# Optimization experiments

Measured on AMD Instinct MI355X. Metric: run time of the kernel, lower is better.

## Reference

```python
import jax, jax.numpy as jnp
import numpy as np

N_NODES = 40000
N_EDGES = 640000
HIDDEN = 128
N_LAYERS = 4
N_CLASSES = 40
SCALING = HIDDEN ** -0.5  # num_heads = 1 -> head_dim = HIDDEN


def setup_inputs() -> dict:
    key = jax.random.key(0)
    ks = jax.random.split(key, 8)
    w_scale = HIDDEN ** -0.5
    h = jax.random.normal(ks[0], (N_NODES, HIDDEN), dtype=jnp.float32)
    src = jax.random.randint(ks[1], (N_EDGES,), 0, N_NODES, dtype=jnp.int32)
    dst = jnp.sort(jax.random.randint(ks[2], (N_EDGES,), 0, N_NODES, dtype=jnp.int32))
    Wq = jax.random.normal(ks[3], (N_LAYERS, HIDDEN, HIDDEN), dtype=jnp.float32) * w_scale
    Wk = jax.random.normal(ks[4], (N_LAYERS, HIDDEN, HIDDEN), dtype=jnp.float32) * w_scale
    Wv = jax.random.normal(ks[5], (N_LAYERS, HIDDEN, HIDDEN), dtype=jnp.float32) * w_scale
    bq = jnp.zeros((N_LAYERS, HIDDEN), dtype=jnp.float32)
    bk = jnp.zeros((N_LAYERS, HIDDEN), dtype=jnp.float32)
    bv = jnp.zeros((N_LAYERS, HIDDEN), dtype=jnp.float32)
    Wout = jax.random.normal(ks[6], (HIDDEN, N_CLASSES), dtype=jnp.float32) * w_scale
    bout = jnp.zeros((N_CLASSES,), dtype=jnp.float32)
    return {"h": h, "src": src, "dst": dst, "Wq": Wq, "bq": bq, "Wk": Wk,
            "bk": bk, "Wv": Wv, "bv": bv, "Wout": Wout, "bout": bout}


def _edge_softmax_spmm(q, k, v, src, dst):
    """Sparse MHA over graph edges (num_heads=1).
    score_e = <q[dst_e], k[src_e]>, softmax over incoming edges per dst,
    out[i] = sum_{e: dst_e = i} attn_e * v[src_e].
    """
    # SDDMM: [E]
    score = jnp.einsum('ed,ed->e', q[dst], k[src])
    # edge softmax over destination segments (stable)
    m = jax.ops.segment_max(score, dst, num_segments=N_NODES)  # [N]
    e = jnp.exp(score - m[dst])                                # [E]
    s = jax.ops.segment_sum(e, dst, num_segments=N_NODES)      # [N]
    attn = e / jnp.maximum(s[dst], 1e-20)                      # [E]
    # SpMM: [N, d]
    return jax.ops.segment_sum(attn[:, None] * v[src], dst, num_segments=N_NODES)


def reference(h, src, dst, Wq, bq, Wk, bk, Wv, bv, Wout, bout):
    for l in range(N_LAYERS):
        q = (h @ Wq[l] + bq[l]) * SCALING
        k = h @ Wk[l] + bk[l]
        v = h @ Wv[l] + bv[l]
        h = _edge_softmax_spmm(q, k, v, src, dst)
    logits = h @ Wout + bout
    return jax.nn.log_softmax(logits, axis=-1)
```

## Files before the change

kernel.cpp:

```cpp
#include <hip/hip_runtime.h>
#include <math.h>

#define N_NODES 40000
#define N_EDGES 640000
#define HIDDEN 128
#define N_LAYERS 4
#define N_CLASSES 40
#define SCALING 0.08838834764831845f

typedef __attribute__((ext_vector_type(8))) short short8;
typedef __attribute__((ext_vector_type(4))) float floatx4;

static __device__ __forceinline__ float b2f(unsigned short u) {
  return __uint_as_float(((unsigned)u) << 16);
}
static __device__ __forceinline__ unsigned short f2b(float f) {
  unsigned u = __float_as_uint(f);
  u += 0x7fff + ((u >> 16) & 1);
  return (unsigned short)(u >> 16);
}

struct MMJob {
  const float* A; const float* B;
  float* Cf; unsigned short* Cb;
  float scale;
  int abt; int ncolsB; int storeT; int padrows;
};
struct MM7 { MMJob j[7]; };
struct MM3 { MMJob j[3]; };

static __device__ __forceinline__ void run_job(const MMJob J, int bi) {
  int ty = threadIdx.x >> 7;
  int c  = threadIdx.x & 127;
  int r  = bi * 2 + ty;
  float acc = 0.f;
  if (J.abt) {
    const float* ar = J.A + (size_t)r * 128;
    const float* br = J.B + (size_t)c * 128;
    #pragma unroll 4
    for (int j = 0; j < 128; ++j) acc += ar[j] * br[j];
  } else if (c < J.ncolsB) {
    const float* ar = J.A + (size_t)r * 128;
    #pragma unroll 4
    for (int j = 0; j < 128; ++j) acc += ar[j] * J.B[(size_t)j * J.ncolsB + c];
  }
  acc *= J.scale;
  if (J.storeT) {
    if (c < J.ncolsB) {
      if (J.Cb) J.Cb[(size_t)c * 128 + r] = f2b(acc);
      else      J.Cf[(size_t)c * 128 + r] = acc;
    } else if (c < J.padrows && J.Cb) {
      J.Cb[(size_t)c * 128 + r] = 0;
    }
  } else if (c < J.ncolsB) {
    if (J.Cb) J.Cb[(size_t)r * J.ncolsB + c] = f2b(acc);
    else      J.Cf[(size_t)r * J.ncolsB + c] = acc;
  }
}

__global__ __launch_bounds__(256) void setup_fold1(
    const float* __restrict__ h_in, const int* __restrict__ dst,
    const float* __restrict__ bq, const float* __restrict__ Wk,
    unsigned short* __restrict__ g0, int* __restrict__ row_start,
    float* __restrict__ zb, MM7 st)
{
  int blk = blockIdx.x;
  if (blk < 2657) {
    int idx = blk * 256 + threadIdx.x;
    if (idx < 640000) {
      const float4* p = (const float4*)h_in + (size_t)idx * 2;
      float4 a = p[0], b = p[1];
      union { unsigned short us[8]; uint4 v; } o;
      o.us[0] = f2b(a.x); o.us[1] = f2b(a.y); o.us[2] = f2b(a.z); o.us[3] = f2b(a.w);
      o.us[4] = f2b(b.x); o.us[5] = f2b(b.y); o.us[6] = f2b(b.z); o.us[7] = f2b(b.w);
      ((uint4*)g0)[idx] = o.v;
      return;
    }
    int c = idx - 640000;
    if (c <= N_NODES) {
      int lo = 0, hi = N_EDGES;
      while (lo < hi) {
        int mid = (lo + hi) >> 1;
        if (dst[mid] < c) lo = mid + 1; else hi = mid;
      }
      row_start[c] = lo;
    }
    return;
  }
  if (blk < 3105) {
    int b2 = blk - 2657;
    run_job(st.j[b2 >> 6], b2 & 63);
    return;
  }
  int t = threadIdx.x;
  if (t < 128) {
    const float* wkr = Wk + (size_t)t * 128;
    float s = 0.f;
    #pragma unroll 4
    for (int o = 0; o < 128; ++o) s += bq[o] * wkr[o];
    zb[t] = s * SCALING;
  }
}

__global__ __launch_bounds__(256) void fold2(MM7 st) {
  run_job(st.j[blockIdx.x >> 6], blockIdx.x & 63);
}

__global__ __launch_bounds__(256) void fold3_z0(
    MM3 st,
    const float* __restrict__ Wq, const float* __restrict__ Wk,
    const float* __restrict__ Wv, const float* __restrict__ Wout,
    const float* __restrict__ bq, const float* __restrict__ bv,
    const float* __restrict__ bout,
    const float* __restrict__ D01, const float* __restrict__ C3f,
    float* __restrict__ zb, float* __restrict__ bout2,
    const unsigned short* __restrict__ g, const unsigned short* __restrict__ WZ0,
    unsigned short* __restrict__ zout)
{
  int blk = blockIdx.x;
  if (blk < 192) {
    run_job(st.j[blk >> 6], blk & 63);
    return;
  }
  if (blk == 192) {
    int t = threadIdx.x;
    __shared__ float cb[128], v1[128], v2[128], cbn[128];
    if (t < 128) cb[t] = bv[t];
    __syncthreads();
    for (int l = 1; l < 4; ++l) {
      const float* Cvl = (l == 1) ? Wv : (l == 2 ? D01 : C3f);
      if (t < 128) {
        float s = bq[(size_t)l * 128 + t];
        for (int o = 0; o < 128; ++o) s += cb[o] * Wq[(size_t)l * 16384 + (size_t)o * 128 + t];
        v1[t] = s;
      }
      __syncthreads();
      if (t < 128) {
        float s = 0.f;
        const float* wkr = Wk + (size_t)l * 16384 + (size_t)t * 128;
        for (int o = 0; o < 128; ++o) s += v1[o] * wkr[o];
        v2[t] = s;
      }
      __syncthreads();
      if (t < 128) {
        float s = 0.f;
        const float* cvr = Cvl + (size_t)t * 128;
        for (int d = 0; d < 128; ++d) s += v2[d] * cvr[d];
        zb[(size_t)l * 128 + t] = s * SCALING;
        float s2 = bv[(size_t)l * 128 + t];
        for (int d = 0; d < 128; ++d) s2 += cb[d] * Wv[(size_t)l * 16384 + (size_t)d * 128 + t];
        cbn[t] = s2;
      }
      __syncthreads();
      if (t < 128) cb[t] = cbn[t];
      __syncthreads();
    }
    if (t < N_CLASSES) {
      float s = bout[t];
      for (int d = 0; d < 128; ++d) s += cb[d] * Wout[(size_t)d * N_CLASSES + t];
      bout2[t] = s;
    }
    return;
  }

  {
    const int tile = blk - 193;
    constexpr int ROWB = 256;
    __shared__ __align__(16) unsigned char cs[32 * ROWB];

    const int tid = threadIdx.x;
    const int wid = tid >> 6, lane = tid & 63;
    const int r = lane & 15, kg = lane >> 4;
    const int colhalf = wid & 1, rowsub = wid >> 1;
    const int colbase = colhalf * 64;
    const int ro = rowsub * 16 + r;
    const int row = tile * 32 + ro;

    short8 hf[4];
    #pragma unroll
    for (int kc = 0; kc < 4; ++kc)
      hf[kc] = *(const short8*)(g + (size_t)row * 128 + kc * 32 + kg * 8);

    floatx4 acc[4];
    #pragma unroll
    for (int df = 0; df < 4; ++df) acc[df] = (floatx4){0.f, 0.f, 0.f, 0.f};

    const unsigned short* wp = WZ0 + (size_t)(colbase + r) * 128 + kg * 8;
    #pragma unroll
    for (int df = 0; df < 4; ++df) {
      #pragma unroll
      for (int kc = 0; kc < 4; ++kc) {
        short8 wf = *(const short8*)(wp + df * 2048 + kc * 32);
        acc[df] = __builtin_amdgcn_mfma_f32_16x16x32_bf16(wf, hf[kc], acc[df], 0, 0, 0);
      }
    }

    #pragma unroll
    for (int df = 0; df < 4; ++df) {
      float4 b4 = *(const float4*)&zb[colbase + df * 16 + kg * 4];
      union { unsigned short us[4]; uint2 u2; } o;
      o.us[0] = f2b(acc[df][0] + b4.x);
      o.us[1] = f2b(acc[df][1] + b4.y);
      o.us[2] = f2b(acc[df][2] + b4.z);
      o.us[3] = f2b(acc[df][3] + b4.w);
      int colb = (colbase + df * 16 + kg * 4) * 2;
      *(uint2*)(cs + ro * ROWB + (colb ^ ((ro & 7) << 4))) = o.u2;
    }
    __syncthreads();

    unsigned char* dstb = (unsigned char*)(zout + (size_t)tile * 32 * 128);
    #pragma unroll
    for (int i = 0; i < 2; ++i) {
      int byte = (i * 256 + tid) * 16;
      int ro2 = byte / ROWB;
      int colb2 = byte & (ROWB - 1);
      *(uint4*)(dstb + byte) =
          *(const uint4*)(cs + ro2 * ROWB + (colb2 ^ ((ro2 & 7) << 4)));
    }
  }
}

__global__ __launch_bounds__(256) void gemm_z(
    const unsigned short* __restrict__ A,
    const unsigned short* __restrict__ Wt,
    const float* __restrict__ bias,
    unsigned short* __restrict__ C)
{
  constexpr int ROWB = 256;
  __shared__ __align__(16) unsigned char cs[32 * ROWB];

  const int tid = threadIdx.x;
  const int wid = tid >> 6, lane = tid & 63;
  const int r = lane & 15, kg = lane >> 4;
  const int colhalf = wid & 1, rowsub = wid >> 1;
  const int colbase = colhalf * 64;
  const int ro = rowsub * 16 + r;
  const int row = blockIdx.x * 32 + ro;

  short8 hf[4];
  #pragma unroll
  for (int kc = 0; kc < 4; ++kc)
    hf[kc] = *(const short8*)(A + (size_t)row * 128 + kc * 32 + kg * 8);

  floatx4 acc[4];
  #pragma unroll
  for (int df = 0; df < 4; ++df) acc[df] = (floatx4){0.f, 0.f, 0.f, 0.f};

  const unsigned short* wp = Wt + (size_t)(colbase + r) * 128 + kg * 8;
  #pragma unroll
  for (int df = 0; df < 4; ++df) {
    #pragma unroll
    for (int kc = 0; kc < 4; ++kc) {
      short8 wf = *(const short8*)(wp + df * 2048 + kc * 32);
      acc[df] = __builtin_amdgcn_mfma_f32_16x16x32_bf16(wf, hf[kc], acc[df], 0, 0, 0);
    }
  }

  #pragma unroll
  for (int df = 0; df < 4; ++df) {
    float4 b4 = *(const float4*)&bias[colbase + df * 16 + kg * 4];
    union { unsigned short us[4]; uint2 u2; } o;
    o.us[0] = f2b(acc[df][0] + b4.x);
    o.us[1] = f2b(acc[df][1] + b4.y);
    o.us[2] = f2b(acc[df][2] + b4.z);
    o.us[3] = f2b(acc[df][3] + b4.w);
    int colb = (colbase + df * 16 + kg * 4) * 2;
    *(uint2*)(cs + ro * ROWB + (colb ^ ((ro & 7) << 4))) = o.u2;
  }
  __syncthreads();

  unsigned char* dstb = (unsigned char*)(C + (size_t)blockIdx.x * 32 * 128);
  #pragma unroll
  for (int i = 0; i < 2; ++i) {
    int byte = (i * 256 + tid) * 16;
    int ro2 = byte / ROWB;
    int colb2 = byte & (ROWB - 1);
    *(uint4*)(dstb + byte) =
        *(const uint4*)(cs + ro2 * ROWB + (colb2 ^ ((ro2 & 7) << 4)));
  }
}

#define EDGE_LOADG(VLD, HF, C)                                          \
  {                                                                     \
    int e_ = (C) + sg;                                                  \
    VLD = e_ < r1;                                                      \
    int s_ = VLD ? src[e_] : 0;                                         \
    HF = *(const short8*)(g + ((size_t)s_ << 7) + sl * 8);              \
  }

#define EDGE_COMPG(VLD, HF)                                             \
  {                                                                     \
    float hd_[8];                                                       \
    _Pragma("unroll")                                                   \
    for (int j = 0; j < 8; ++j) hd_[j] = b2f((unsigned short)HF[j]);    \
    float d0_ = 0.f, d1_ = 0.f;                                         \
    _Pragma("unroll")                                                   \
    for (int j = 0; j < 4; ++j) d0_ += qd[j] * hd_[j];                  \
    _Pragma("unroll")                                                   \
    for (int j = 4; j < 8; ++j) d1_ += qd[j] * hd_[j];                  \
    float d_ = d0_ + d1_;                                               \
    d_ += __shfl_xor(d_, 1, 64);                                        \
    d_ += __shfl_xor(d_, 2, 64);                                        \
    d_ += __shfl_xor(d_, 4, 64);                                        \
    d_ += __shfl_xor(d_, 8, 64);                                        \
    float w_ = VLD ? __expf(d_) : 0.f;                                  \
    ws += w_;                                                           \
    _Pragma("unroll")                                                   \
    for (int j = 0; j < 8; ++j) acc[j] += w_ * hd_[j];                  \
  }

#define EDGE_BODY                                                       \
  float acc[8] = {0.f, 0.f, 0.f, 0.f, 0.f, 0.f, 0.f, 0.f};              \
  float ws = 0.f;                                                       \
  bool vA, vB;                                                          \
  short8 hA, hB;                                                        \
  EDGE_LOADG(vA, hA, r0);                                               \
  EDGE_LOADG(vB, hB, r0 + 4);                                           \
  for (int c = r0; c < r1; c += 8) {                                    \
    bool vC, vD;                                                        \
    short8 hC, hD;                                                      \
    EDGE_LOADG(vC, hC, c + 8);                                          \
    EDGE_LOADG(vD, hD, c + 12);                                         \
    EDGE_COMPG(vA, hA);                                                 \
    EDGE_COMPG(vB, hB);                                                 \
    vA = vC; hA = hC;                                                   \
    vB = vD; hB = hD;                                                   \
  }                                                                     \
  _Pragma("unroll")                                                     \
  for (int off = 16; off <= 32; off <<= 1) {                            \
    ws += __shfl_xor(ws, off, 64);                                      \
    _Pragma("unroll")                                                   \
    for (int j = 0; j < 8; ++j) acc[j] += __shfl_xor(acc[j], off, 64);  \
  }

__global__ __launch_bounds__(128) void edge_fused(
    const unsigned short* __restrict__ z, const unsigned short* __restrict__ g,
    const int* __restrict__ src, const int* __restrict__ row_start,
    unsigned short* __restrict__ gout)
{
  const int lane = threadIdx.x & 63;
  const int node = blockIdx.x * 2 + (threadIdx.x >> 6);
  const int sg = lane >> 4, sl = lane & 15;

  short8 qf = *(const short8*)(z + ((size_t)node << 7) + sl * 8);
  float qd[8];
  #pragma unroll
  for (int j = 0; j < 8; ++j) qd[j] = b2f((unsigned short)qf[j]);

  const int r0 = row_start[node], r1 = row_start[node + 1];

  EDGE_BODY

  if (sg == 0) {
    float inv = (ws > 1e-20f) ? 1.0f / ws : 0.0f;
    union { unsigned short us[8]; uint4 u4; } o;
    #pragma unroll
    for (int j = 0; j < 8; ++j) o.us[j] = f2b(acc[j] * inv);
    *(uint4*)(gout + (size_t)node * 128 + sl * 8) = o.u4;
  }
}

__global__ __launch_bounds__(128) void edge_head(
    const unsigned short* __restrict__ z, const unsigned short* __restrict__ g,
    const int* __restrict__ src, const int* __restrict__ row_start,
    const unsigned short* __restrict__ WOt, const float* __restrict__ bout2,
    float* __restrict__ out)
{
  const int lane = threadIdx.x & 63;
  const int node = blockIdx.x * 2 + (threadIdx.x >> 6);
  const int sg = lane >> 4, sl = lane & 15;

  short8 qf = *(const short8*)(z + ((size_t)node << 7) + sl * 8);
  float qd[8];
  #pragma unroll
  for (int j = 0; j < 8; ++j) qd[j] = b2f((unsigned short)qf[j]);

  const int r0 = row_start[node], r1 = row_start[node + 1];

  EDGE_BODY

  float inv = (ws > 1e-20f) ? 1.0f / ws : 0.0f;

  float cls[10];
  #pragma unroll
  for (int it = 0; it < 10; ++it) {
    int c = sg * 10 + it;
    short8 w = *(const short8*)(WOt + (size_t)c * 128 + sl * 8);
    float p = 0.f;
    #pragma unroll
    for (int j = 0; j < 8; ++j) p += acc[j] * b2f((unsigned short)w[j]);
    p += __shfl_xor(p, 1, 64);
    p += __shfl_xor(p, 2, 64);
    p += __shfl_xor(p, 4, 64);
    p += __shfl_xor(p, 8, 64);
    cls[it] = p * inv + bout2[c];
  }
  float m = cls[0];
  #pragma unroll
  for (int it = 1; it < 10; ++it) m = fmaxf(m, cls[it]);
  m = fmaxf(m, __shfl_xor(m, 16, 64));
  m = fmaxf(m, __shfl_xor(m, 32, 64));
  float s = 0.f;
  #pragma unroll
  for (int it = 0; it < 10; ++it) s += __expf(cls[it] - m);
  s += __shfl_xor(s, 16, 64);
  s += __shfl_xor(s, 32, 64);
  float lse = m + logf(s);

  if (sl < 10) {
    float v = cls[0];
    #pragma unroll
    for (int it = 1; it < 10; ++it) if (sl == it) v = cls[it];
    out[(size_t)node * N_CLASSES + sg * 10 + sl] = v - lse;
  }
}

#undef EDGE_BODY
#undef EDGE_COMPG
#undef EDGE_LOADG

extern "C" void kernel_launch(void* const* d_in, const int* in_sizes, int n_in,
                              void* d_out, int out_size, void* d_ws, size_t ws_size,
                              hipStream_t stream) {
  const float* h_in = (const float*)d_in[0];
  const int*   src  = (const int*)d_in[1];
  const int*   dst  = (const int*)d_in[2];
  const float* Wq   = (const float*)d_in[3];
  const float* bq   = (const float*)d_in[4];
  const float* Wk   = (const float*)d_in[5];
  const float* bk   = (const float*)d_in[6];
  const float* Wv   = (const float*)d_in[7];
  const float* bv   = (const float*)d_in[8];
  const float* Wout = (const float*)d_in[9];
  const float* bout = (const float*)d_in[10];
  float* out = (float*)d_out;
  (void)bk;

  char* ws = (char*)d_ws;
  size_t off = 0;
  auto alloc = [&](size_t bytes) -> void* {
    void* p = ws + off;
    off += (bytes + 255) & ~(size_t)255;
    return p;
  };
  int*            row_start = (int*)           alloc((size_t)(N_NODES + 1) * sizeof(int));
  unsigned short* g0        = (unsigned short*)alloc((size_t)N_NODES * 128 * 2);
  unsigned short* g1        = (unsigned short*)alloc((size_t)N_NODES * 128 * 2);
  unsigned short* zbuf      = (unsigned short*)alloc((size_t)N_NODES * 128 * 2);
  unsigned short* WZ        = (unsigned short*)alloc((size_t)4 * 16384 * 2);
  unsigned short* WOt       = (unsigned short*)alloc((size_t)48 * 128 * 2);
  float*          D01  = (float*)alloc(16384 * 4);
  float*          D23  = (float*)alloc(16384 * 4);
  float*          A1f  = (float*)alloc(16384 * 4);
  float*          B1f  = (float*)alloc(16384 * 4);
  float*          E3   = (float*)alloc(16384 * 4);
  float*          F3   = (float*)alloc(16384 * 4);
  float*          A2f  = (float*)alloc(16384 * 4);
  float*          B2f  = (float*)alloc(16384 * 4);
  float*          A3f  = (float*)alloc(16384 * 4);
  float*          B3f  = (float*)alloc(16384 * 4);
  float*          C4f  = (float*)alloc(16384 * 4);
  float*          C3f  = (float*)alloc(16384 * 4);
  float*          zb   = (float*)alloc(4 * 128 * 4);
  float*          bout2 = (float*)alloc(64 * 4);

  auto J = [](const float* A, const float* B, float* Cf, unsigned short* Cb,
              float scale, int abt, int ncolsB, int storeT, int padrows) {
    MMJob j; j.A = A; j.B = B; j.Cf = Cf; j.Cb = Cb; j.scale = scale;
    j.abt = abt; j.ncolsB = ncolsB; j.storeT = storeT; j.padrows = padrows;
    return j;
  };
  const float* Wq_l[4] = {Wq, Wq + 16384, Wq + 32768, Wq + 49152};
  const float* Wk_l[4] = {Wk, Wk + 16384, Wk + 32768, Wk + 49152};
  const float* Wv_l[4] = {Wv, Wv + 16384, Wv + 32768, Wv + 49152};

  MM7 s1;
  s1.j[0] = J(Wk_l[0], Wq_l[0], nullptr, WZ, SCALING, 1, 128, 0, 0);
  s1.j[1] = J(Wv_l[0], Wv_l[1], D01, nullptr, 1.f, 0, 128, 0, 0);
  s1.j[2] = J(Wv_l[2], Wv_l[3], D23, nullptr, 1.f, 0, 128, 0, 0);
  s1.j[3] = J(Wv_l[0], Wk_l[1], A1f, nullptr, 1.f, 0, 128, 0, 0);
  s1.j[4] = J(Wv_l[0], Wq_l[1], B1f, nullptr, 1.f, 0, 128, 0, 0);
  s1.j[5] = J(Wv_l[2], Wk_l[3], E3,  nullptr, 1.f, 0, 128, 0, 0);
  s1.j[6] = J(Wv_l[2], Wq_l[3], F3,  nullptr, 1.f, 0, 128, 0, 0);

  MM7 s2;
  s2.j[0] = J(A1f, B1f, nullptr, WZ + 16384, SCALING, 1, 128, 0, 0);
  s2.j[1] = J(D01, Wk_l[2], A2f, nullptr, 1.f, 0, 128, 0, 0);
  s2.j[2] = J(D01, Wq_l[2], B2f, nullptr, 1.f, 0, 128, 0, 0);
  s2.j[3] = J(D01, E3, A3f, nullptr, 1.f, 0, 128, 0, 0);
  s2.j[4] = J(D01, F3, B3f, nullptr, 1.f, 0, 128, 0, 0);
  s2.j[5] = J(D01, D23, C4f, nullptr, 1.f, 0, 128, 0, 0);
  s2.j[6] = J(D01, Wv_l[2], C3f, nullptr, 1.f, 0, 128, 0, 0);

  MM3 s3;
  s3.j[0] = J(A2f, B2f, nullptr, WZ + 32768, SCALING, 1, 128, 0, 0);
  s3.j[1] = J(A3f, B3f, nullptr, WZ + 49152, SCALING, 1, 128, 0, 0);
  s3.j[2] = J(C4f, Wout, nullptr, WOt, 1.f, 0, N_CLASSES, 1, 48);

  setup_fold1<<<3106, 256, 0, stream>>>(h_in, dst, bq, Wk, g0, row_start, zb, s1);
  fold2<<<448, 256, 0, stream>>>(s2);
  fold3_z0<<<1443, 256, 0, stream>>>(s3, Wq, Wk, Wv, Wout, bq, bv, bout,
                                     D01, C3f, zb, bout2, g0, WZ, zbuf);

  edge_fused<<<N_NODES / 2, 128, 0, stream>>>(zbuf, g0, src, row_start, g1);
  gemm_z<<<1250, 256, 0, stream>>>(g1, WZ + 16384, zb + 128, zbuf);
  edge_fused<<<N_NODES / 2, 128, 0, stream>>>(zbuf, g1, src, row_start, g0);
  gemm_z<<<1250, 256, 0, stream>>>(g0, WZ + 32768, zb + 256, zbuf);
  edge_fused<<<N_NODES / 2, 128, 0, stream>>>(zbuf, g0, src, row_start, g1);
  gemm_z<<<1250, 256, 0, stream>>>(g1, WZ + 49152, zb + 384, zbuf);
  edge_head<<<N_NODES / 2, 128, 0, stream>>>(zbuf, g1, src, row_start, WOt, bout2, out);
}
```

Baseline: 241.5 us.

## Split output head into separate MFMA kernel and fold log2e into scores

Replaces the fused edge_head kernel, which did the per-node 128x40 output projection with scalar dot products and shuffles, with a plain edge_fused pass followed by a separate MFMA bf16 GEMM kernel that also computes log-softmax and writes through shared memory. The log2(e) factor is folded into the score-projection scales so the edge kernel can call exp2f instead of __expf. This costs one extra kernel launch and a bf16 round trip of the final hidden state through global memory. In exchange the class projection moves onto matrix cores and the edge loop does slightly less work per edge.

```diff
diff --git a/kernel.cpp b/kernel.cpp
--- a/kernel.cpp
+++ b/kernel.cpp
@@ -7,6 +7,7 @@
 #define N_LAYERS 4
 #define N_CLASSES 40
 #define SCALING 0.08838834764831845f
+#define LOG2E 1.4426950408889634f
 
 typedef __attribute__((ext_vector_type(8))) short short8;
 typedef __attribute__((ext_vector_type(4))) float floatx4;
@@ -98,7 +99,7 @@
     float s = 0.f;
     #pragma unroll 4
     for (int o = 0; o < 128; ++o) s += bq[o] * wkr[o];
-    zb[t] = s * SCALING;
+    zb[t] = s * (SCALING * LOG2E);
   }
 }
 
@@ -146,7 +147,7 @@
         float s = 0.f;
         const float* cvr = Cvl + (size_t)t * 128;
         for (int d = 0; d < 128; ++d) s += v2[d] * cvr[d];
-        zb[(size_t)l * 128 + t] = s * SCALING;
+        zb[(size_t)l * 128 + t] = s * (SCALING * LOG2E);
         float s2 = bv[(size_t)l * 128 + t];
         for (int d = 0; d < 128; ++d) s2 += cb[d] * Wv[(size_t)l * 16384 + (size_t)d * 128 + t];
         cbn[t] = s2;
@@ -280,7 +281,26 @@
   }
 }
 
-#define EDGE_LOADG(VLD, HF, C)                                          \
+__global__ __launch_bounds__(128) void edge_fused(
+    const unsigned short* __restrict__ z, const unsigned short* __restrict__ g,
+    const int* __restrict__ src, const int* __restrict__ row_start,
+    unsigned short* __restrict__ gout)
+{
+  const int lane = threadIdx.x & 63;
+  const int node = blockIdx.x * 2 + (threadIdx.x >> 6);
+  const int sg = lane >> 4, sl = lane & 15;
+
+  short8 qf = *(const short8*)(z + ((size_t)node << 7) + sl * 8);
+  float qd[8];
+  #pragma unroll
+  for (int j = 0; j < 8; ++j) qd[j] = b2f((unsigned short)qf[j]);
+
+  const int r0 = row_start[node], r1 = row_start[node + 1];
+
+  float acc[8] = {0.f, 0.f, 0.f, 0.f, 0.f, 0.f, 0.f, 0.f};
+  float ws = 0.f;
+
+#define LOADG(VLD, HF, C)                                               \
   {                                                                     \
     int e_ = (C) + sg;                                                  \
     VLD = e_ < r1;                                                      \
@@ -288,7 +308,7 @@
     HF = *(const short8*)(g + ((size_t)s_ << 7) + sl * 8);              \
   }
 
-#define EDGE_COMPG(VLD, HF)                                             \
+#define COMPG(VLD, HF)                                                  \
   {                                                                     \
     float hd_[8];                                                       \
     _Pragma("unroll")                                                   \
@@ -303,53 +323,37 @@
     d_ += __shfl_xor(d_, 2, 64);                                        \
     d_ += __shfl_xor(d_, 4, 64);                                        \
     d_ += __shfl_xor(d_, 8, 64);                                        \
-    float w_ = VLD ? __expf(d_) : 0.f;                                  \
+    float w_ = VLD ? exp2f(d_) : 0.f;                                   \
     ws += w_;                                                           \
     _Pragma("unroll")                                                   \
     for (int j = 0; j < 8; ++j) acc[j] += w_ * hd_[j];                  \
   }
 
-#define EDGE_BODY                                                       \
-  float acc[8] = {0.f, 0.f, 0.f, 0.f, 0.f, 0.f, 0.f, 0.f};              \
-  float ws = 0.f;                                                       \
-  bool vA, vB;                                                          \
-  short8 hA, hB;                                                        \
-  EDGE_LOADG(vA, hA, r0);                                               \
-  EDGE_LOADG(vB, hB, r0 + 4);                                           \
-  for (int c = r0; c < r1; c += 8) {                                    \
-    bool vC, vD;                                                        \
-    short8 hC, hD;                                                      \
-    EDGE_LOADG(vC, hC, c + 8);                                          \
-    EDGE_LOADG(vD, hD, c + 12);                                         \
-    EDGE_COMPG(vA, hA);                                                 \
-    EDGE_COMPG(vB, hB);                                                 \
-    vA = vC; hA = hC;                                                   \
-    vB = vD; hB = hD;                                                   \
-  }                                                                     \
-  _Pragma("unroll")                                                     \
-  for (int off = 16; off <= 32; off <<= 1) {                            \
-    ws += __shfl_xor(ws, off, 64);                                      \
-    _Pragma("unroll")                                                   \
-    for (int j = 0; j < 8; ++j) acc[j] += __shfl_xor(acc[j], off, 64);  \
-  }
-
-__global__ __launch_bounds__(128) void edge_fused(
-    const unsigned short* __restrict__ z, const unsigned short* __restrict__ g,
-    const int* __restrict__ src, const int* __restrict__ row_start,
-    unsigned short* __restrict__ gout)
-{
-  const int lane = threadIdx.x & 63;
-  const int node = blockIdx.x * 2 + (threadIdx.x >> 6);
-  const int sg = lane >> 4, sl = lane & 15;
-
-  short8 qf = *(const short8*)(z + ((size_t)node << 7) + sl * 8);
-  float qd[8];
-  #pragma unroll
-  for (int j = 0; j < 8; ++j) qd[j] = b2f((unsigned short)qf[j]);
-
-  const int r0 = row_start[node], r1 = row_start[node + 1];
-
-  EDGE_BODY
+  bool vA, vB;
+  short8 hA, hB;
+  LOADG(vA, hA, r0);
+  LOADG(vB, hB, r0 + 4);
+
+  for (int c = r0; c < r1; c += 8) {
+    bool vC, vD;
+    short8 hC, hD;
+    LOADG(vC, hC, c + 8);
+    LOADG(vD, hD, c + 12);
+    COMPG(vA, hA);
+    COMPG(vB, hB);
+    vA = vC; hA = hC;
+    vB = vD; hB = hD;
+  }
+
+#undef LOADG
+#undef COMPG
+
+  #pragma unroll
+  for (int off = 16; off <= 32; off <<= 1) {
+    ws += __shfl_xor(ws, off, 64);
+    #pragma unroll
+    for (int j = 0; j < 8; ++j) acc[j] += __shfl_xor(acc[j], off, 64);
+  }
 
   if (sg == 0) {
     float inv = (ws > 1e-20f) ? 1.0f / ws : 0.0f;
@@ -360,64 +364,66 @@
   }
 }
 
-__global__ __launch_bounds__(128) void edge_head(
-    const unsigned short* __restrict__ z, const unsigned short* __restrict__ g,
-    const int* __restrict__ src, const int* __restrict__ row_start,
-    const unsigned short* __restrict__ WOt, const float* __restrict__ bout2,
-    float* __restrict__ out)
+__global__ __launch_bounds__(256) void out_head_mfma(
+    const unsigned short* __restrict__ h, const unsigned short* __restrict__ wout_t,
+    const float* __restrict__ bout, float* __restrict__ out)
 {
-  const int lane = threadIdx.x & 63;
-  const int node = blockIdx.x * 2 + (threadIdx.x >> 6);
-  const int sg = lane >> 4, sl = lane & 15;
-
-  short8 qf = *(const short8*)(z + ((size_t)node << 7) + sl * 8);
-  float qd[8];
-  #pragma unroll
-  for (int j = 0; j < 8; ++j) qd[j] = b2f((unsigned short)qf[j]);
-
-  const int r0 = row_start[node], r1 = row_start[node + 1];
-
-  EDGE_BODY
-
-  float inv = (ws > 1e-20f) ? 1.0f / ws : 0.0f;
-
-  float cls[10];
-  #pragma unroll
-  for (int it = 0; it < 10; ++it) {
-    int c = sg * 10 + it;
-    short8 w = *(const short8*)(WOt + (size_t)c * 128 + sl * 8);
-    float p = 0.f;
-    #pragma unroll
-    for (int j = 0; j < 8; ++j) p += acc[j] * b2f((unsigned short)w[j]);
-    p += __shfl_xor(p, 1, 64);
-    p += __shfl_xor(p, 2, 64);
-    p += __shfl_xor(p, 4, 64);
-    p += __shfl_xor(p, 8, 64);
-    cls[it] = p * inv + bout2[c];
-  }
-  float m = cls[0];
-  #pragma unroll
-  for (int it = 1; it < 10; ++it) m = fmaxf(m, cls[it]);
-  m = fmaxf(m, __shfl_xor(m, 16, 64));
-  m = fmaxf(m, __shfl_xor(m, 32, 64));
-  float s = 0.f;
-  #pragma unroll
-  for (int it = 0; it < 10; ++it) s += __expf(cls[it] - m);
-  s += __shfl_xor(s, 16, 64);
-  s += __shfl_xor(s, 32, 64);
-  float lse = m + logf(s);
-
-  if (sl < 10) {
-    float v = cls[0];
-    #pragma unroll
-    for (int it = 1; it < 10; ++it) if (sl == it) v = cls[it];
-    out[(size_t)node * N_CLASSES + sg * 10 + sl] = v - lse;
-  }
-}
-
-#undef EDGE_BODY
-#undef EDGE_COMPG
-#undef EDGE_LOADG
+  __shared__ __align__(16) float os[64 * N_CLASSES];
+
+  const int wid = threadIdx.x >> 6, lane = threadIdx.x & 63;
+  const int r = lane & 15, kg = lane >> 4;
+  const int row_base = blockIdx.x * 64 + wid * 16;
+  const int ar = row_base + r;
+
+  floatx4 acc[3];
+  #pragma unroll
+  for (int n = 0; n < 3; ++n) acc[n] = (floatx4){0.f, 0.f, 0.f, 0.f};
+
+  const unsigned short* ap = h + (size_t)ar * 128 + kg * 8;
+  const unsigned short* bp = wout_t + (size_t)r * 128 + kg * 8;
+
+  #pragma unroll
+  for (int kc = 0; kc < 128; kc += 32) {
+    short8 a0 = *(const short8*)(ap + kc);
+    #pragma unroll
+    for (int n = 0; n < 3; ++n) {
+      short8 b = *(const short8*)(bp + n * 2048 + kc);
+      acc[n] = __builtin_amdgcn_mfma_f32_16x16x32_bf16(a0, b, acc[n], 0, 0, 0);
+    }
+  }
+
+  float bn0 = bout[r];
+  float bn1 = bout[16 + r];
+  float bn2 = (r < 8) ? bout[32 + r] : 0.f;
+
+  #pragma unroll
+  for (int g = 0; g < 4; ++g) {
+    int rl = wid * 16 + kg * 4 + g;
+    float l0 = acc[0][g] + bn0;
+    float l1 = acc[1][g] + bn1;
+    float l2 = acc[2][g] + bn2;
+    float m = fmaxf(l0, l1);
+    if (r < 8) m = fmaxf(m, l2);
+    #pragma unroll
+    for (int off = 8; off >= 1; off >>= 1) m = fmaxf(m, __shfl_xor(m, off, 64));
+    float s = __expf(l0 - m) + __expf(l1 - m) + ((r < 8) ? __expf(l2 - m) : 0.f);
+    #pragma unroll
+    for (int off = 8; off >= 1; off >>= 1) s += __shfl_xor(s, off, 64);
+    float lse = m + logf(s);
+    os[rl * N_CLASSES + r]      = l0 - lse;
+    os[rl * N_CLASSES + 16 + r] = l1 - lse;
+    if (r < 8) os[rl * N_CLASSES + 32 + r] = l2 - lse;
+  }
+  __syncthreads();
+
+  float* dstb = out + (size_t)blockIdx.x * 64 * N_CLASSES;
+  #pragma unroll
+  for (int i = 0; i < 3; ++i) {
+    int idx = i * 256 + threadIdx.x;
+    if (idx < 640)
+      *(uint4*)(dstb + idx * 4) = *(const uint4*)(os + idx * 4);
+  }
+}
 
 extern "C" void kernel_launch(void* const* d_in, const int* in_sizes, int n_in,
                               void* d_out, int out_size, void* d_ws, size_t ws_size,
@@ -474,8 +480,10 @@
   const float* Wk_l[4] = {Wk, Wk + 16384, Wk + 32768, Wk + 49152};
   const float* Wv_l[4] = {Wv, Wv + 16384, Wv + 32768, Wv + 49152};
 
+  const float ZSC = SCALING * LOG2E;
+
   MM7 s1;
-  s1.j[0] = J(Wk_l[0], Wq_l[0], nullptr, WZ, SCALING, 1, 128, 0, 0);
+  s1.j[0] = J(Wk_l[0], Wq_l[0], nullptr, WZ, ZSC, 1, 128, 0, 0);
   s1.j[1] = J(Wv_l[0], Wv_l[1], D01, nullptr, 1.f, 0, 128, 0, 0);
   s1.j[2] = J(Wv_l[2], Wv_l[3], D23, nullptr, 1.f, 0, 128, 0, 0);
   s1.j[3] = J(Wv_l[0], Wk_l[1], A1f, nullptr, 1.f, 0, 128, 0, 0);
@@ -484,7 +492,7 @@
   s1.j[6] = J(Wv_l[2], Wq_l[3], F3,  nullptr, 1.f, 0, 128, 0, 0);
 
   MM7 s2;
-  s2.j[0] = J(A1f, B1f, nullptr, WZ + 16384, SCALING, 1, 128, 0, 0);
+  s2.j[0] = J(A1f, B1f, nullptr, WZ + 16384, ZSC, 1, 128, 0, 0);
   s2.j[1] = J(D01, Wk_l[2], A2f, nullptr, 1.f, 0, 128, 0, 0);
   s2.j[2] = J(D01, Wq_l[2], B2f, nullptr, 1.f, 0, 128, 0, 0);
   s2.j[3] = J(D01, E3, A3f, nullptr, 1.f, 0, 128, 0, 0);
@@ -493,8 +501,8 @@
   s2.j[6] = J(D01, Wv_l[2], C3f, nullptr, 1.f, 0, 128, 0, 0);
 
   MM3 s3;
-  s3.j[0] = J(A2f, B2f, nullptr, WZ + 32768, SCALING, 1, 128, 0, 0);
-  s3.j[1] = J(A3f, B3f, nullptr, WZ + 49152, SCALING, 1, 128, 0, 0);
+  s3.j[0] = J(A2f, B2f, nullptr, WZ + 32768, ZSC, 1, 128, 0, 0);
+  s3.j[1] = J(A3f, B3f, nullptr, WZ + 49152, ZSC, 1, 128, 0, 0);
   s3.j[2] = J(C4f, Wout, nullptr, WOt, 1.f, 0, N_CLASSES, 1, 48);
 
   setup_fold1<<<3106, 256, 0, stream>>>(h_in, dst, bq, Wk, g0, row_start, zb, s1);
@@ -508,5 +516,6 @@
   gemm_z<<<1250, 256, 0, stream>>>(g0, WZ + 32768, zb + 256, zbuf);
   edge_fused<<<N_NODES / 2, 128, 0, stream>>>(zbuf, g0, src, row_start, g1);
   gemm_z<<<1250, 256, 0, stream>>>(g1, WZ + 49152, zb + 384, zbuf);
-  edge_head<<<N_NODES / 2, 128, 0, stream>>>(zbuf, g1, src, row_start, WOt, bout2, out);
-}
+  edge_fused<<<N_NODES / 2, 128, 0, stream>>>(zbuf, g1, src, row_start, g0);
+  out_head_mfma<<<625, 256, 0, stream>>>(g0, WOt, bout2, out);
+}
```

After: 238.6 us. Within noise of the previous version (-1.2%).
